# Optimization experiments

Measured on AMD Instinct MI355X. Metric: run time of the kernel, lower is better.

The kernel has to match this reference:

```python
import jax, jax.numpy as jnp
import numpy as np

N_HEAD = 16


def setup_inputs() -> dict:
    B, T, C, H = 64, 128, 2048, N_HEAD
    hd = C // H
    key = jax.random.key(0)
    ks = jax.random.split(key, 5)
    x = jax.random.normal(ks[0], (B, T, C), dtype=jnp.float32)
    wq = jax.random.normal(ks[1], (C, C), dtype=jnp.float32) * 0.02
    wk = jax.random.normal(ks[2], (C, C), dtype=jnp.float32) * 0.02
    wv = jax.random.normal(ks[3], (C, C), dtype=jnp.float32) * 0.02
    wo = jax.random.normal(ks[4], (C, C), dtype=jnp.float32) * 0.02
    # RoPE frequencies: freqs_cis = exp(i * pos * theta_j), theta_j = 10000^(-2j/hd)
    pos = jnp.arange(T, dtype=jnp.float32)
    inv_freq = 1.0 / (10000.0 ** (jnp.arange(0, hd, 2, dtype=jnp.float32) / hd))  # [hd/2]
    ang = pos[:, None] * inv_freq[None, :]  # [T, hd/2]
    return {
        "x": x,
        "freqs_cos": jnp.cos(ang),
        "freqs_sin": jnp.sin(ang),
        "wq": wq, "wk": wk, "wv": wv, "wo": wo,
    }


def _apply_rope(t, cos, sin):
    # t: [B,T,H,hd]; complex multiply on interleaved (even, odd) pairs
    B, T, H, hd = t.shape
    tr = t.reshape(B, T, H, hd // 2, 2)
    te, to = tr[..., 0], tr[..., 1]
    c = cos[None, :, None, :]  # [1,T,1,hd/2]
    s = sin[None, :, None, :]
    oe = te * c - to * s
    oo = te * s + to * c
    return jnp.stack([oe, oo], axis=-1).reshape(B, T, H, hd)


def reference(x, freqs_cos, freqs_sin, wq, wk, wv, wo):
    B, T, C = x.shape
    H = N_HEAD
    hd = C // H
    q = (x @ wq.T).reshape(B, T, H, hd)
    k = (x @ wk.T).reshape(B, T, H, hd)
    v = (x @ wv.T).reshape(B, T, H, hd)
    q = _apply_rope(q, freqs_cos, freqs_sin)
    k = _apply_rope(k, freqs_cos, freqs_sin)
    # scores: [B,H,T,S]
    scores = jnp.einsum("bthd,bshd->bhts", q, k) / (hd ** 0.5)
    causal = jnp.tril(jnp.ones((T, T), dtype=bool))
    scores = jnp.where(causal[None, None], scores, jnp.float32(-jnp.inf))
    probs = jax.nn.softmax(scores, axis=-1)  # dropout is identity in eval
    out = jnp.einsum("bhts,bshd->bthd", probs, v).reshape(B, T, C)
    return out @ wo.T
```

## Files before the change

kernel.cpp:

```cpp
#include <hip/hip_runtime.h>
#include <cstdint>


typedef unsigned short ushort;
typedef __bf16 bf16x8 __attribute__((ext_vector_type(8)));
typedef float floatx4 __attribute__((ext_vector_type(4)));

__device__ __forceinline__ ushort f2bf(float f) {
  union { float f; uint32_t u; } v; v.f = f;
  uint32_t r = v.u + 0x7FFFu + ((v.u >> 16) & 1u);
  return (ushort)(r >> 16);
}
__device__ __forceinline__ float bf2f(ushort h) {
  union { uint32_t u; float f; } v; v.u = ((uint32_t)h) << 16;
  return v.f;
}

__device__ __forceinline__ void load_lds16(const void* g, void* l) {
  __builtin_amdgcn_global_load_lds(
      (__attribute__((address_space(1))) void*)(uintptr_t)g,
      (__attribute__((address_space(3))) void*)(uint32_t)(uintptr_t)l,
      16, 0, 0);
}

__device__ __forceinline__ void store_out(ushort* C, size_t i, float v) { C[i] = f2bf(v); }
__device__ __forceinline__ void store_out(float* C, size_t i, float v) { C[i] = v; }

__device__ __forceinline__ void phase_mid() {
  __builtin_amdgcn_s_barrier();
  asm volatile("s_waitcnt lgkmcnt(0)" ::: "memory");
  __builtin_amdgcn_sched_barrier(0);
}
__device__ __forceinline__ void phase_end() {
  __builtin_amdgcn_s_barrier();
  __builtin_amdgcn_sched_barrier(0);
}

template <typename OutT>
__device__ __forceinline__ void gemm256_body(const ushort* __restrict__ A,
                                             const ushort* __restrict__ B,
                                             OutT* __restrict__ C,
                                             int M, int N, int K) {
  (void)M;
  __shared__ __align__(16) ushort As[2][256 * 64];
  __shared__ __align__(16) ushort Bs[2][256 * 64];
  const int tid = threadIdx.x;
  const int wave = tid >> 6, lane = tid & 63;
  const int quad = lane >> 4, colv = lane & 15;
  const int wm = wave & 1, wn = wave >> 1;
  const int m0 = blockIdx.x * 256, n0 = blockIdx.y * 256;

  const int a_base = (wm * 128 + colv) * 64;
  const int b_base = (wn * 64 + colv) * 64;
  const int kg0 = ((quad) ^ (colv & 7)) << 3;
  const int kg1 = ((quad | 4) ^ (colv & 7)) << 3;

  const int srow = tid >> 3;
  const int scol = ((tid & 7) ^ (srow & 7)) << 3;
  const ushort* Ag = A + (size_t)(m0 + srow) * K + scol;
  const ushort* Bg = B + (size_t)(n0 + srow) * K + scol;
  const int ldsw = wave * 512;

  floatx4 acc[8][4] = {};
  bf16x8 af[4][2], bfr[4][2];

#define STAGE(Gb, T, half, kt)                                             \
  {                                                                        \
    const ushort* g_ = (Gb) + (size_t)((half) * 128) * K + (kt) * 64;      \
    load_lds16(g_, &(T)[(half) * 8192 + ldsw]);                            \
    load_lds16(g_ + (size_t)64 * K, &(T)[(half) * 8192 + 4096 + ldsw]);    \
  }

#define READ_B_ALL(bi)                                                     \
  _Pragma("unroll") for (int nf = 0; nf < 4; ++nf) {                       \
    bfr[nf][0] = *(const bf16x8*)&Bs[bi][b_base + nf * 1024 + kg0];        \
    bfr[nf][1] = *(const bf16x8*)&Bs[bi][b_base + nf * 1024 + kg1];        \
  }

#define READ_A(bi, off)                                                    \
  _Pragma("unroll") for (int mf = 0; mf < 4; ++mf) {                       \
    af[mf][0] = *(const bf16x8*)&As[bi][a_base + (off) + mf * 1024 + kg0]; \
    af[mf][1] = *(const bf16x8*)&As[bi][a_base + (off) + mf * 1024 + kg1]; \
  }

#define MFMA16(ks, mo)                                                     \
  __builtin_amdgcn_s_setprio(1);                                           \
  _Pragma("unroll") for (int mf = 0; mf < 4; ++mf)                         \
  _Pragma("unroll") for (int nf = 0; nf < 4; ++nf)                         \
    acc[(mo) + mf][nf] = __builtin_amdgcn_mfma_f32_16x16x32_bf16(          \
        af[mf][(ks)], bfr[nf][(ks)], acc[(mo) + mf][nf], 0, 0, 0);         \
  __builtin_amdgcn_s_setprio(0);

  STAGE(Bg, Bs[0], 0, 0)
  STAGE(Bg, Bs[0], 1, 0)
  STAGE(Ag, As[0], 0, 0)
  STAGE(Ag, As[0], 1, 0)
  STAGE(Bg, Bs[1], 0, 1)
  STAGE(Bg, Bs[1], 1, 1)
  STAGE(Ag, As[1], 0, 1)
  asm volatile("s_waitcnt vmcnt(6)" ::: "memory");
  __builtin_amdgcn_s_barrier();
  __builtin_amdgcn_sched_barrier(0);

  const int NT = K >> 6;
#pragma unroll 1
  for (int it = 0; it < (NT >> 1); ++it) {
    const int s0 = (2 * it + 2 < NT) ? 2 * it + 2 : NT - 1;
    const int s1 = (2 * it + 3 < NT) ? 2 * it + 3 : NT - 1;

    READ_B_ALL(0)
    READ_A(0, 0)
    STAGE(Ag, As[1], 1, 2 * it + 1)
    phase_mid();
    MFMA16(0, 0)
    phase_end();
    STAGE(Bg, Bs[0], 0, s0)
    phase_mid();
    MFMA16(1, 0)
    phase_end();
    READ_A(0, 4096)
    STAGE(Bg, Bs[0], 1, s0)
    phase_mid();
    MFMA16(0, 4)
    phase_end();
    STAGE(Ag, As[0], 0, s0)
    asm volatile("s_waitcnt vmcnt(6)" ::: "memory");
    phase_mid();
    MFMA16(1, 4)
    phase_end();
    READ_B_ALL(1)
    READ_A(1, 0)
    STAGE(Ag, As[0], 1, s0)
    phase_mid();
    MFMA16(0, 0)
    phase_end();
    STAGE(Bg, Bs[1], 0, s1)
    phase_mid();
    MFMA16(1, 0)
    phase_end();
    READ_A(1, 4096)
    STAGE(Bg, Bs[1], 1, s1)
    phase_mid();
    MFMA16(0, 4)
    phase_end();
    STAGE(Ag, As[1], 0, s1)
    asm volatile("s_waitcnt vmcnt(6)" ::: "memory");
    phase_mid();
    MFMA16(1, 4)
    phase_end();
  }
  asm volatile("s_waitcnt vmcnt(0)" ::: "memory");

#pragma unroll
  for (int mf = 0; mf < 8; ++mf)
#pragma unroll
    for (int nf = 0; nf < 4; ++nf)
#pragma unroll
      for (int r = 0; r < 4; ++r) {
        int m = m0 + wm * 128 + mf * 16 + quad * 4 + r;
        int n = n0 + wn * 64 + nf * 16 + colv;
        store_out(C, (size_t)m * N + n, acc[mf][nf][r]);
      }
#undef STAGE
#undef READ_B_ALL
#undef READ_A
#undef MFMA16
}

__global__ __launch_bounds__(512) void gemm_qkv(
    const ushort* __restrict__ A, const ushort* __restrict__ Wq,
    const ushort* __restrict__ Wk, const ushort* __restrict__ Wv,
    ushort* __restrict__ Q, ushort* __restrict__ Kb, ushort* __restrict__ V) {
  const ushort* B = (blockIdx.z == 0) ? Wq : (blockIdx.z == 1) ? Wk : Wv;
  ushort* C = (blockIdx.z == 0) ? Q : (blockIdx.z == 1) ? Kb : V;
  gemm256_body<ushort>(A, B, C, 8192, 2048, 2048);
}

__global__ __launch_bounds__(512) void gemm_out_k(
    const ushort* __restrict__ A, const ushort* __restrict__ B,
    float* __restrict__ C) {
  gemm256_body<float>(A, B, C, 8192, 2048, 2048);
}

#define NX 4194304u
#define NW 1048576u
__global__ void cvt_all(const float* __restrict__ x, const float* __restrict__ wq,
                        const float* __restrict__ wk, const float* __restrict__ wv,
                        const float* __restrict__ wo,
                        ushort* __restrict__ xb, ushort* __restrict__ wqb,
                        ushort* __restrict__ wkb, ushort* __restrict__ wvb,
                        ushort* __restrict__ wob) {
  uint32_t i = blockIdx.x * 256u + threadIdx.x;
  const float* src;
  ushort* dst;
  uint32_t off;
  if (i < NX) {
    src = x; dst = xb; off = i;
  } else {
    uint32_t i2 = i - NX;
    uint32_t r = i2 >> 20;
    off = i2 & (NW - 1u);
    src = (r == 0) ? wq : (r == 1) ? wk : (r == 2) ? wv : wo;
    dst = (r == 0) ? wqb : (r == 1) ? wkb : (r == 2) ? wvb : wob;
  }
  float4 v = ((const float4*)src)[off];
  ushort4 o;
  o.x = f2bf(v.x); o.y = f2bf(v.y); o.z = f2bf(v.z); o.w = f2bf(v.w);
  ((ushort4*)dst)[off] = o;
}

__global__ __launch_bounds__(256) void attn_kernel(
    const ushort* __restrict__ Q, const ushort* __restrict__ K,
    const ushort* __restrict__ V, const float* __restrict__ Cf,
    const float* __restrict__ Sf, ushort* __restrict__ O) {
  __shared__ __align__(16) ushort Qs[128 * 128];
  __shared__ __align__(16) ushort KVs[128 * 128];
  const int b = blockIdx.x >> 4, h = blockIdx.x & 15;
  const int tid = threadIdx.x, wave = tid >> 6, lane = tid & 63;
  const int quad = lane >> 4, colv = lane & 15;
  const size_t gbase = (size_t)b * 262144 + (size_t)h * 128;

#pragma unroll
  for (int sgi = 0; sgi < 8; ++sgi) {
    int seg = tid + sgi * 256;
    int t = seg >> 4, g = seg & 15;
    uint4 qv = *(const uint4*)(Q + gbase + (size_t)t * 2048 + g * 8);
    uint4 kv = *(const uint4*)(K + gbase + (size_t)t * 2048 + g * 8);
    float4 cf = *(const float4*)(Cf + t * 64 + g * 4);
    float4 sf = *(const float4*)(Sf + t * 64 + g * 4);
    uint32_t* qw = (uint32_t*)&qv;
    uint32_t* kw = (uint32_t*)&kv;
#pragma unroll
    for (int j = 0; j < 4; ++j) {
      float c = (&cf.x)[j], s = (&sf.x)[j];
      uint32_t w = qw[j];
      float e = bf2f((ushort)(w & 0xFFFF)), o = bf2f((ushort)(w >> 16));
      qw[j] = (uint32_t)f2bf(e * c - o * s) | ((uint32_t)f2bf(e * s + o * c) << 16);
      w = kw[j];
      e = bf2f((ushort)(w & 0xFFFF)); o = bf2f((ushort)(w >> 16));
      kw[j] = (uint32_t)f2bf(e * c - o * s) | ((uint32_t)f2bf(e * s + o * c) << 16);
    }
    int so = t * 128 + ((g ^ (t & 15)) << 3);
    *(uint4*)&Qs[so] = qv;
    *(uint4*)&KVs[so] = kv;
  }
  __syncthreads();

  floatx4 accs[2][8] = {};
#pragma unroll
  for (int kc = 0; kc < 4; ++kc) {
    bf16x8 af[2], bfr[8];
#pragma unroll
    for (int i = 0; i < 2; ++i) {
      int r = wave * 32 + i * 16 + colv;
      af[i] = *(const bf16x8*)&Qs[r * 128 + ((((kc << 2) | quad) ^ (r & 15)) << 3)];
    }
#pragma unroll
    for (int j = 0; j < 8; ++j) {
      int r = j * 16 + colv;
      bfr[j] = *(const bf16x8*)&KVs[r * 128 + ((((kc << 2) | quad) ^ (r & 15)) << 3)];
    }
#pragma unroll
    for (int i = 0; i < 2; ++i)
#pragma unroll
      for (int j = 0; j < 8; ++j)
        accs[i][j] = __builtin_amdgcn_mfma_f32_16x16x32_bf16(af[i], bfr[j], accs[i][j], 0, 0, 0);
  }

  const float scale = 0.08838834764831845f;
#pragma unroll
  for (int i = 0; i < 2; ++i)
#pragma unroll
    for (int r = 0; r < 4; ++r) {
      int t = wave * 32 + i * 16 + quad * 4 + r;
      float mx = -1e30f;
#pragma unroll
      for (int j = 0; j < 8; ++j) {
        int s = j * 16 + colv;
        float v = accs[i][j][r] * scale;
        v = (s <= t) ? v : -1e30f;
        accs[i][j][r] = v;
        mx = fmaxf(mx, v);
      }
#pragma unroll
      for (int off = 1; off < 16; off <<= 1) mx = fmaxf(mx, __shfl_xor(mx, off, 64));
      float l = 0.f;
#pragma unroll
      for (int j = 0; j < 8; ++j) {
        float p = __expf(accs[i][j][r] - mx);
        accs[i][j][r] = p;
        l += p;
      }
#pragma unroll
      for (int off = 1; off < 16; off <<= 1) l += __shfl_xor(l, off, 64);
      float inv = 1.0f / l;
#pragma unroll
      for (int j = 0; j < 8; ++j) {
        int s = j * 16 + colv;
        Qs[t * 128 + ((((s >> 3) ^ (t & 15)) << 3) | (s & 7))] = f2bf(accs[i][j][r] * inv);
      }
    }
  __syncthreads();

#pragma unroll
  for (int sgi = 0; sgi < 8; ++sgi) {
    int seg = tid + sgi * 256;
    int t = seg >> 4;
    int dg = (seg & 15) << 3;
    uint4 vv = *(const uint4*)(V + gbase + (size_t)t * 2048 + dg);
    const ushort* vp = (const ushort*)&vv;
#pragma unroll
    for (int jj = 0; jj < 8; ++jj) {
      int d = dg + jj;
      KVs[d * 128 + ((((t >> 3) ^ (d & 15)) << 3) | (t & 7))] = vp[jj];
    }
  }
  __syncthreads();

  floatx4 acco[2][8] = {};
#pragma unroll
  for (int kc = 0; kc < 4; ++kc) {
    bf16x8 af[2], bfr[8];
#pragma unroll
    for (int i = 0; i < 2; ++i) {
      int r = wave * 32 + i * 16 + colv;
      af[i] = *(const bf16x8*)&Qs[r * 128 + ((((kc << 2) | quad) ^ (r & 15)) << 3)];
    }
#pragma unroll
    for (int j = 0; j < 8; ++j) {
      int r = j * 16 + colv;
      bfr[j] = *(const bf16x8*)&KVs[r * 128 + ((((kc << 2) | quad) ^ (r & 15)) << 3)];
    }
#pragma unroll
    for (int i = 0; i < 2; ++i)
#pragma unroll
      for (int j = 0; j < 8; ++j)
        acco[i][j] = __builtin_amdgcn_mfma_f32_16x16x32_bf16(af[i], bfr[j], acco[i][j], 0, 0, 0);
  }

#pragma unroll
  for (int i = 0; i < 2; ++i)
#pragma unroll
    for (int j = 0; j < 8; ++j)
#pragma unroll
      for (int r = 0; r < 4; ++r) {
        int t = wave * 32 + i * 16 + quad * 4 + r;
        int d = j * 16 + colv;
        O[gbase + (size_t)t * 2048 + d] = f2bf(acco[i][j][r]);
      }
}

extern "C" void kernel_launch(void* const* d_in, const int* in_sizes, int n_in,
                              void* d_out, int out_size, void* d_ws, size_t ws_size,
                              hipStream_t stream) {
  const float* x    = (const float*)d_in[0];
  const float* fcos = (const float*)d_in[1];
  const float* fsin = (const float*)d_in[2];
  const float* wq   = (const float*)d_in[3];
  const float* wk   = (const float*)d_in[4];
  const float* wv   = (const float*)d_in[5];
  const float* wo   = (const float*)d_in[6];
  float* out = (float*)d_out;

  const size_t CC = 2048ull * 2048ull;
  const size_t MC = 8192ull * 2048ull;
  ushort* wob = (ushort*)d_ws;
  ushort* xb  = wob + CC;
  ushort* wqb = xb + MC;
  ushort* wkb = wqb + CC;
  ushort* wvb = wkb + CC;
  ushort* Qb  = wvb + CC;
  ushort* Kb  = Qb + MC;
  ushort* Vb  = Kb + MC;

  unsigned cvt_blocks = (unsigned)((MC + 4 * CC) / 4 / 256);
  cvt_all<<<dim3(cvt_blocks), 256, 0, stream>>>(x, wq, wk, wv, wo, xb, wqb, wkb, wvb, wob);

  gemm_qkv<<<dim3(32, 8, 3), 512, 0, stream>>>(xb, wqb, wkb, wvb, Qb, Kb, Vb);
  attn_kernel<<<dim3(1024), 256, 0, stream>>>(Qb, Kb, Vb, fcos, fsin, xb);
  gemm_out_k<<<dim3(32, 8), 512, 0, stream>>>(xb, wob, out);
}
```

Baseline: 448.2 us.

## Split GEMM LDS fragment reads per k-slice and prefetch V in attention

The GEMM main loop now issues LDS reads of A/B fragments per k-substep instead of all at once. This interleaves them more finely with the MFMA phases and reshuffles where global staging and the vmcnt waits sit. The attention kernel loads V into registers alongside Q/K at the start and transposes it into LDS during softmax, removing a separate global load phase and one barrier. It also raises MFMA wave priority and sets launch bounds for 2 blocks per CU. The costs are higher register pressure from holding V, and a changed vmcnt accounting that must still match the outstanding loads.

```diff
diff --git a/kernel.cpp b/kernel.cpp
--- a/kernel.cpp
+++ b/kernel.cpp
@@ -71,17 +71,13 @@
     load_lds16(g_ + (size_t)64 * K, &(T)[(half) * 8192 + 4096 + ldsw]);    \
   }
 
-#define READ_B_ALL(bi)                                                     \
-  _Pragma("unroll") for (int nf = 0; nf < 4; ++nf) {                       \
-    bfr[nf][0] = *(const bf16x8*)&Bs[bi][b_base + nf * 1024 + kg0];        \
-    bfr[nf][1] = *(const bf16x8*)&Bs[bi][b_base + nf * 1024 + kg1];        \
-  }
-
-#define READ_A(bi, off)                                                    \
-  _Pragma("unroll") for (int mf = 0; mf < 4; ++mf) {                       \
-    af[mf][0] = *(const bf16x8*)&As[bi][a_base + (off) + mf * 1024 + kg0]; \
-    af[mf][1] = *(const bf16x8*)&As[bi][a_base + (off) + mf * 1024 + kg1]; \
-  }
+#define READ_B_KS(bi, ks, kg)                                              \
+  _Pragma("unroll") for (int nf = 0; nf < 4; ++nf)                         \
+    bfr[nf][ks] = *(const bf16x8*)&Bs[bi][b_base + nf * 1024 + (kg)];
+
+#define READ_A_KS(bi, off, ks, kg)                                         \
+  _Pragma("unroll") for (int mf = 0; mf < 4; ++mf)                         \
+    af[mf][ks] = *(const bf16x8*)&As[bi][a_base + (off) + mf * 1024 + (kg)];
 
 #define MFMA16(ks, mo)                                                     \
   __builtin_amdgcn_s_setprio(1);                                           \
@@ -108,41 +104,47 @@
     const int s0 = (2 * it + 2 < NT) ? 2 * it + 2 : NT - 1;
     const int s1 = (2 * it + 3 < NT) ? 2 * it + 3 : NT - 1;
 
-    READ_B_ALL(0)
-    READ_A(0, 0)
+    READ_B_KS(0, 0, kg0)
+    READ_A_KS(0, 0, 0, kg0)
     STAGE(Ag, As[1], 1, 2 * it + 1)
     phase_mid();
     MFMA16(0, 0)
     phase_end();
+    READ_B_KS(0, 1, kg1)
+    READ_A_KS(0, 0, 1, kg1)
+    phase_mid();
+    MFMA16(1, 0)
+    phase_end();
+    READ_A_KS(0, 4096, 0, kg0)
+    READ_A_KS(0, 4096, 1, kg1)
     STAGE(Bg, Bs[0], 0, s0)
     phase_mid();
+    MFMA16(0, 4)
+    phase_end();
+    STAGE(Bg, Bs[0], 1, s0)
+    asm volatile("s_waitcnt vmcnt(4)" ::: "memory");
+    phase_mid();
+    MFMA16(1, 4)
+    phase_end();
+    READ_B_KS(1, 0, kg0)
+    READ_A_KS(1, 0, 0, kg0)
+    STAGE(Ag, As[0], 0, s0)
+    phase_mid();
+    MFMA16(0, 0)
+    phase_end();
+    READ_B_KS(1, 1, kg1)
+    READ_A_KS(1, 0, 1, kg1)
+    STAGE(Ag, As[0], 1, s0)
+    phase_mid();
     MFMA16(1, 0)
     phase_end();
-    READ_A(0, 4096)
-    STAGE(Bg, Bs[0], 1, s0)
+    READ_A_KS(1, 4096, 0, kg0)
+    READ_A_KS(1, 4096, 1, kg1)
+    STAGE(Bg, Bs[1], 0, s1)
     phase_mid();
     MFMA16(0, 4)
     phase_end();
-    STAGE(Ag, As[0], 0, s0)
-    asm volatile("s_waitcnt vmcnt(6)" ::: "memory");
-    phase_mid();
-    MFMA16(1, 4)
-    phase_end();
-    READ_B_ALL(1)
-    READ_A(1, 0)
-    STAGE(Ag, As[0], 1, s0)
-    phase_mid();
-    MFMA16(0, 0)
-    phase_end();
-    STAGE(Bg, Bs[1], 0, s1)
-    phase_mid();
-    MFMA16(1, 0)
-    phase_end();
-    READ_A(1, 4096)
     STAGE(Bg, Bs[1], 1, s1)
-    phase_mid();
-    MFMA16(0, 4)
-    phase_end();
     STAGE(Ag, As[1], 0, s1)
     asm volatile("s_waitcnt vmcnt(6)" ::: "memory");
     phase_mid();
@@ -162,8 +164,8 @@
         store_out(C, (size_t)m * N + n, acc[mf][nf][r]);
       }
 #undef STAGE
-#undef READ_B_ALL
-#undef READ_A
+#undef READ_B_KS
+#undef READ_A_KS
 #undef MFMA16
 }
 
@@ -209,7 +211,7 @@
   ((ushort4*)dst)[off] = o;
 }
 
-__global__ __launch_bounds__(256) void attn_kernel(
+__global__ __launch_bounds__(256, 2) void attn_kernel(
     const ushort* __restrict__ Q, const ushort* __restrict__ K,
     const ushort* __restrict__ V, const float* __restrict__ Cf,
     const float* __restrict__ Sf, ushort* __restrict__ O) {
@@ -220,12 +222,14 @@
   const int quad = lane >> 4, colv = lane & 15;
   const size_t gbase = (size_t)b * 262144 + (size_t)h * 128;
 
+  uint4 vreg[8];
 #pragma unroll
   for (int sgi = 0; sgi < 8; ++sgi) {
     int seg = tid + sgi * 256;
     int t = seg >> 4, g = seg & 15;
     uint4 qv = *(const uint4*)(Q + gbase + (size_t)t * 2048 + g * 8);
     uint4 kv = *(const uint4*)(K + gbase + (size_t)t * 2048 + g * 8);
+    vreg[sgi] = *(const uint4*)(V + gbase + (size_t)t * 2048 + g * 8);
     float4 cf = *(const float4*)(Cf + t * 64 + g * 4);
     float4 sf = *(const float4*)(Sf + t * 64 + g * 4);
     uint32_t* qw = (uint32_t*)&qv;
@@ -260,11 +264,27 @@
       int r = j * 16 + colv;
       bfr[j] = *(const bf16x8*)&KVs[r * 128 + ((((kc << 2) | quad) ^ (r & 15)) << 3)];
     }
+    __builtin_amdgcn_s_setprio(1);
 #pragma unroll
     for (int i = 0; i < 2; ++i)
 #pragma unroll
       for (int j = 0; j < 8; ++j)
         accs[i][j] = __builtin_amdgcn_mfma_f32_16x16x32_bf16(af[i], bfr[j], accs[i][j], 0, 0, 0);
+    __builtin_amdgcn_s_setprio(0);
+  }
+  __syncthreads();
+
+#pragma unroll
+  for (int sgi = 0; sgi < 8; ++sgi) {
+    int seg = tid + sgi * 256;
+    int t = seg >> 4;
+    int dg = (seg & 15) << 3;
+    const ushort* vp = (const ushort*)&vreg[sgi];
+#pragma unroll
+    for (int jj = 0; jj < 8; ++jj) {
+      int d = dg + jj;
+      KVs[d * 128 + ((((t >> 3) ^ (d & 15)) << 3) | (t & 7))] = vp[jj];
+    }
   }
 
   const float scale = 0.08838834764831845f;
@@ -302,21 +322,6 @@
     }
   __syncthreads();
 
-#pragma unroll
-  for (int sgi = 0; sgi < 8; ++sgi) {
-    int seg = tid + sgi * 256;
-    int t = seg >> 4;
-    int dg = (seg & 15) << 3;
-    uint4 vv = *(const uint4*)(V + gbase + (size_t)t * 2048 + dg);
-    const ushort* vp = (const ushort*)&vv;
-#pragma unroll
-    for (int jj = 0; jj < 8; ++jj) {
-      int d = dg + jj;
-      KVs[d * 128 + ((((t >> 3) ^ (d & 15)) << 3) | (t & 7))] = vp[jj];
-    }
-  }
-  __syncthreads();
-
   floatx4 acco[2][8] = {};
 #pragma unroll
   for (int kc = 0; kc < 4; ++kc) {
@@ -331,11 +336,13 @@
       int r = j * 16 + colv;
       bfr[j] = *(const bf16x8*)&KVs[r * 128 + ((((kc << 2) | quad) ^ (r & 15)) << 3)];
     }
+    __builtin_amdgcn_s_setprio(1);
 #pragma unroll
     for (int i = 0; i < 2; ++i)
 #pragma unroll
       for (int j = 0; j < 8; ++j)
         acco[i][j] = __builtin_amdgcn_mfma_f32_16x16x32_bf16(af[i], bfr[j], acco[i][j], 0, 0, 0);
+    __builtin_amdgcn_s_setprio(0);
   }
 
 #pragma unroll
```

After: 450.4 us. No clear change (+0.5%).
